# Performance work log

Measured on AMD Instinct MI355X. Metric: run time of the kernel, lower is better.

## Reference

```python
import jax, jax.numpy as jnp
import numpy as np
import math

B, S, NV, D, VD = 2, 1024, 256, 4096, 768
H, KV, HD = 32, 4, 128
REP = H // KV
THETA, YSCALE, YALPHA, YBETA = 10000.0, 40.0, 1.0, 32.0
MAXSEQ = 2048
NEG = -1e30


def _yarn_cos_sin(n_pos):
    # YaRN-scaled RoPE tables, faithful to precompute_rope_yarn
    L_full = MAXSEQ * int(YSCALE)  # max_seq_len * yarn_scale as in __init__
    inv_freq = 1.0 / THETA ** (np.arange(0, HD, 2, dtype=np.float32) / HD)
    wavelengths = 2.0 * math.pi / inv_freq
    r = L_full / wavelengths
    gamma = np.clip((r - YALPHA) / (YBETA - YALPHA), 0.0, 1.0)
    inv_freq = inv_freq * ((1.0 - gamma) / YSCALE + gamma)
    freqs = np.outer(np.arange(n_pos, dtype=np.float32), inv_freq)
    emb = np.concatenate([freqs, freqs], axis=-1) / math.sqrt(0.1 * math.log(YSCALE) + 1.0)
    return jnp.asarray(np.cos(emb), jnp.float32), jnp.asarray(np.sin(emb), jnp.float32)


def setup_inputs() -> dict:
    key = jax.random.key(0)
    ks = jax.random.split(key, 7)
    x = jax.random.normal(ks[0], (B, S, D), jnp.float32)
    vision_features = jax.random.normal(ks[1], (B, NV, VD), jnp.float32)
    wq = jax.random.normal(ks[2], (H * HD, D), jnp.float32) * 0.02
    wk = jax.random.normal(ks[3], (KV * HD, D), jnp.float32) * 0.02
    wv = jax.random.normal(ks[4], (KV * HD, D), jnp.float32) * 0.02
    wo = jax.random.normal(ks[5], (D, H * HD), jnp.float32) * 0.02
    w_vision_kv = jax.random.normal(ks[6], (2 * KV * HD, VD), jnp.float32) * 0.02
    cos, sin = _yarn_cos_sin(S + NV)
    return {"x": x, "vision_features": vision_features, "wq": wq, "wk": wk,
            "wv": wv, "wo": wo, "w_vision_kv": w_vision_kv, "cos": cos, "sin": sin}


def _rotate_half(t):
    t1, t2 = t[..., : HD // 2], t[..., HD // 2 :]
    return jnp.concatenate([-t2, t1], axis=-1)


def reference(x, vision_features, wq, wk, wv, wo, w_vision_kv, cos, sin):
    b, s, _ = x.shape
    q = (x @ wq.T).reshape(b, s, H, HD)
    k = (x @ wk.T).reshape(b, s, KV, HD)
    v = (x @ wv.T).reshape(b, s, KV, HD)
    # vision KV prefix
    vkv = vision_features @ w_vision_kv.T  # [b, nv, 2*KV*HD]
    vk, vv = jnp.split(vkv, 2, axis=-1)
    nv = vision_features.shape[1]
    vk = vk.reshape(b, nv, KV, HD)
    vv = vv.reshape(b, nv, KV, HD)
    k = jnp.concatenate([vk, k], axis=1)  # [b, kvlen, KV, HD]
    v = jnp.concatenate([vv, v], axis=1)
    kvlen = k.shape[1]
    # RoPE (positions broadcast over heads)
    cq, sq = cos[None, :s, None, :], sin[None, :s, None, :]
    ck, sk = cos[None, :kvlen, None, :], sin[None, :kvlen, None, :]
    q = q * cq + _rotate_half(q) * sq
    k = k * ck + _rotate_half(k) * sk
    # GQA without materializing repeated K/V: group q heads by kv head
    qg = q.reshape(b, s, KV, REP, HD)
    scores = jnp.einsum("bsgrd,btgd->bgrst", qg, k) * (HD ** -0.5)
    # flash-style bottom-right causal: q pos i sees kv pos j <= i + (kvlen - s)
    i = jnp.arange(s)[:, None]
    j = jnp.arange(kvlen)[None, :]
    mask = j <= i + (kvlen - s)
    scores = jnp.where(mask, scores, NEG)
    probs = jax.nn.softmax(scores, axis=-1)
    out = jnp.einsum("bgrst,btgd->bsgrd", probs, v).reshape(b, s, H * HD)
    return out @ wo.T
```

## Files before the change

kernel.cpp:

```cpp
#include <hip/hip_runtime.h>
#include <hip/hip_bf16.h>
#include <cstdint>
#include <cstddef>

typedef short bf16x8 __attribute__((ext_vector_type(8)));
typedef float f32x4 __attribute__((ext_vector_type(4)));

__device__ __forceinline__ void gload_lds16(const void* g, void* l) {
  __builtin_amdgcn_global_load_lds((__attribute__((address_space(1))) const void*)g,
                                   (__attribute__((address_space(3))) void*)l, 16, 0, 0);
}

__device__ __forceinline__ unsigned short f2bf(float f) {
  unsigned u = __builtin_bit_cast(unsigned, f);
  u += 0x7fffu + ((u >> 16) & 1u);
  return (unsigned short)(u >> 16);
}
__device__ __forceinline__ float bf2f(unsigned short h) {
  unsigned u = ((unsigned)h) << 16;
  return __builtin_bit_cast(float, u);
}

__global__ void k_cast(const float* __restrict__ in, unsigned short* __restrict__ out, int n4) {
  int i = blockIdx.x * blockDim.x + threadIdx.x;
  int stride = gridDim.x * blockDim.x;
  for (; i < n4; i += stride) {
    float4 v = reinterpret_cast<const float4*>(in)[i];
    ushort4 o;
    o.x = f2bf(v.x); o.y = f2bf(v.y); o.z = f2bf(v.z); o.w = f2bf(v.w);
    reinterpret_cast<ushort4*>(out)[i] = o;
  }
}

__device__ __forceinline__ void storeC(float* C, size_t i, float v) { C[i] = v; }
__device__ __forceinline__ void storeC(unsigned short* C, size_t i, float v) { C[i] = f2bf(v); }

template <typename OutT>
__global__ __launch_bounds__(256) void k_gemm_bt(
    const unsigned short* __restrict__ A,
    const unsigned short* __restrict__ B,
    OutT* __restrict__ C,
    int M, int N, int K) {
  __shared__ __align__(16) unsigned short lA[128 * 64];
  __shared__ __align__(16) unsigned short lB[128 * 64];
  const int tid = threadIdx.x;
  const int w = tid >> 6, l = tid & 63;
  const int nwg = gridDim.x * gridDim.y;
  const int orig = blockIdx.y * gridDim.x + blockIdx.x;
  const int cpx = nwg >> 3;
  const int tile = (orig & 7) * cpx + (orig >> 3);
  const int m0 = (tile % gridDim.x) * 128;
  const int n0 = (tile / gridDim.x) * 128;
  const int wm = (w >> 1) * 64, wn = (w & 1) * 64;

  f32x4 acc[4][4];
#pragma unroll
  for (int i = 0; i < 4; ++i)
#pragma unroll
    for (int j = 0; j < 4; ++j) acc[i][j] = f32x4{0.f, 0.f, 0.f, 0.f};

  char* lAc = (char*)lA;
  char* lBc = (char*)lB;

  for (int k0 = 0; k0 < K; k0 += 64) {
#pragma unroll
    for (int p = 0; p < 4; ++p) {
      int r = (w * 4 + p) * 8 + (l >> 3);
      int c = (l & 7) ^ (r & 7);
      gload_lds16(A + (size_t)(m0 + r) * K + k0 + c * 8, lAc + (w * 4 + p) * 1024);
      gload_lds16(B + (size_t)(n0 + r) * K + k0 + c * 8, lBc + (w * 4 + p) * 1024);
    }
    __syncthreads();
#pragma unroll
    for (int kk = 0; kk < 2; ++kk) {
      bf16x8 af[4], bfr[4];
#pragma unroll
      for (int i = 0; i < 4; ++i) {
        int r = wm + i * 16 + (l & 15);
        int slot = (kk * 4 + (l >> 4)) ^ (r & 7);
        af[i] = *(const bf16x8*)(lAc + r * 128 + slot * 16);
      }
#pragma unroll
      for (int j = 0; j < 4; ++j) {
        int r = wn + j * 16 + (l & 15);
        int slot = (kk * 4 + (l >> 4)) ^ (r & 7);
        bfr[j] = *(const bf16x8*)(lBc + r * 128 + slot * 16);
      }
#pragma unroll
      for (int i = 0; i < 4; ++i)
#pragma unroll
        for (int j = 0; j < 4; ++j)
          acc[i][j] = __builtin_amdgcn_mfma_f32_16x16x32_bf16(af[i], bfr[j], acc[i][j], 0, 0, 0);
    }
    __syncthreads();
  }

#pragma unroll
  for (int i = 0; i < 4; ++i)
#pragma unroll
    for (int j = 0; j < 4; ++j) {
      int row = m0 + wm + i * 16 + (l >> 4) * 4;
      int col = n0 + wn + j * 16 + (l & 15);
#pragma unroll
      for (int r = 0; r < 4; ++r)
        storeC(C, (size_t)(row + r) * N + col, acc[i][j][r]);
    }
}

__global__ void k_rope_q(unsigned short* __restrict__ qkv,
                         const float* __restrict__ cosT, const float* __restrict__ sinT) {
  int idx = blockIdx.x * blockDim.x + threadIdx.x;
  if (idx >= 2048 * 32 * 64) return;
  int d0 = idx & 63;
  int h = (idx >> 6) & 31;
  int m = idx >> 11;
  int s = m & 1023;
  unsigned short* row = qkv + (size_t)m * 5120 + h * 128;
  float a = bf2f(row[d0]), b = bf2f(row[d0 + 64]);
  float c0 = cosT[s * 128 + d0], s0 = sinT[s * 128 + d0];
  float c1 = cosT[s * 128 + d0 + 64], s1 = sinT[s * 128 + d0 + 64];
  const float sc = 0.08838834764831845f;
  row[d0] = f2bf((a * c0 - b * s0) * sc);
  row[d0 + 64] = f2bf((b * c1 + a * s1) * sc);
}

__global__ void k_build_k(const unsigned short* __restrict__ qkv,
                          const unsigned short* __restrict__ vkv,
                          const float* __restrict__ cosT, const float* __restrict__ sinT,
                          unsigned short* __restrict__ k_all) {
  int idx = blockIdx.x * blockDim.x + threadIdx.x;
  if (idx >= 8 * 1280 * 64) return;
  int d0 = idx & 63;
  int t = (idx >> 6) % 1280;
  int bg = idx / (64 * 1280);
  int b = bg >> 2, g = bg & 3;
  float a, bb;
  if (t < 256) {
    const unsigned short* src = vkv + (size_t)(b * 256 + t) * 1024 + g * 128;
    a = bf2f(src[d0]); bb = bf2f(src[d0 + 64]);
  } else {
    const unsigned short* src = qkv + (size_t)(b * 1024 + t - 256) * 5120 + 4096 + g * 128;
    a = bf2f(src[d0]); bb = bf2f(src[d0 + 64]);
  }
  float c0 = cosT[t * 128 + d0], s0 = sinT[t * 128 + d0];
  float c1 = cosT[t * 128 + d0 + 64], s1 = sinT[t * 128 + d0 + 64];
  unsigned short* dst = k_all + ((size_t)bg * 1280 + t) * 128;
  dst[d0] = f2bf(a * c0 - bb * s0);
  dst[d0 + 64] = f2bf(bb * c1 + a * s1);
}

__global__ void k_build_v(const unsigned short* __restrict__ qkv,
                          const unsigned short* __restrict__ vkv,
                          unsigned short* __restrict__ v_t) {
  int idx = blockIdx.x * blockDim.x + threadIdx.x;
  if (idx >= 8 * 128 * 1280) return;
  int t = idx % 1280;
  int d = (idx / 1280) & 127;
  int bg = idx / (1280 * 128);
  int b = bg >> 2, g = bg & 3;
  unsigned short v;
  if (t < 256) v = vkv[(size_t)(b * 256 + t) * 1024 + 512 + g * 128 + d];
  else         v = qkv[(size_t)(b * 1024 + t - 256) * 5120 + 4608 + g * 128 + d];
  v_t[(size_t)bg * 128 * 1280 + (size_t)d * 1280 + t] = v;
}

__global__ __launch_bounds__(256) void k_attn(
    const unsigned short* __restrict__ qr,
    const unsigned short* __restrict__ k_all,
    const unsigned short* __restrict__ v_t,
    unsigned short* __restrict__ attn) {
  __shared__ __align__(16) unsigned short lK[2][64 * 128];
  __shared__ __align__(16) unsigned short lV[2][128 * 64];
  __shared__ __align__(16) unsigned short lPT[4][16][64];

  const int tid = threadIdx.x, w = tid >> 6, l = tid & 63;
  const int lq = l & 15, g = l >> 4;
  const int qb = (15 - (int)blockIdx.x) * 64;
  const int h = blockIdx.y, b = blockIdx.z;
  const int bg = b * 4 + (h >> 3);
  const unsigned short* kg = k_all + (size_t)bg * 1280 * 128;
  const unsigned short* vg = v_t + (size_t)bg * 128 * 1280;

  char* lKc = (char*)lK;
  char* lVc = (char*)lV;
  char* pbuf = (char*)&lPT[w][0][0];

  bf16x8 aq[4];
  {
    int row = qb + w * 16 + lq;
    const unsigned short* p = qr + (size_t)(b * 1024 + row) * 5120 + h * 128 + g * 8;
    aq[0] = *(const bf16x8*)(p);
    aq[1] = *(const bf16x8*)(p + 32);
    aq[2] = *(const bf16x8*)(p + 64);
    aq[3] = *(const bf16x8*)(p + 96);
  }

  f32x4 o[8];
#pragma unroll
  for (int i = 0; i < 8; ++i) o[i] = f32x4{0.f, 0.f, 0.f, 0.f};
  float mr = -1e30f;
  float lrp = 0.f;

  const int qrow_l = qb + w * 16 + lq;
  int tlim = qb + 320;
  if (tlim > 1280) tlim = 1280;
  const int nIter = tlim >> 6;

  auto stage = [&](int t0, int bufsel) {
#pragma unroll
    for (int p = 0; p < 4; ++p) {
      int r = (w * 4 + p) * 4 + (l >> 4);
      int c = (l & 15) ^ (r & 7);
      gload_lds16(kg + (size_t)(t0 + r) * 128 + c * 8,
                  lKc + bufsel * 16384 + (w * 4 + p) * 1024);
    }
#pragma unroll
    for (int p = 0; p < 4; ++p) {
      int d = (w * 4 + p) * 8 + (l >> 3);
      int c = (l & 7) ^ (d & 7);
      gload_lds16(vg + (size_t)d * 1280 + t0 + c * 8,
                  lVc + bufsel * 16384 + (w * 4 + p) * 1024);
    }
  };

  stage(0, 0);
  __syncthreads();

  int buf = 0;
  for (int it = 0; it < nIter; ++it) {
    const int t0 = it << 6;
    if (it + 1 < nIter) stage(t0 + 64, buf ^ 1);

    const char* kbase = lKc + buf * 16384;
    const char* vbase = lVc + buf * 16384;

    f32x4 sT[4];
#pragma unroll
    for (int sub = 0; sub < 4; ++sub) {
      f32x4 s4 = {0.f, 0.f, 0.f, 0.f};
      int krow = sub * 16 + lq;
      const char* kb = kbase + krow * 256;
#pragma unroll
      for (int kk = 0; kk < 4; ++kk) {
        int slot = (kk * 4 + g) ^ (krow & 7);
        bf16x8 kf = *(const bf16x8*)(kb + slot * 16);
        s4 = __builtin_amdgcn_mfma_f32_16x16x32_bf16(kf, aq[kk], s4, 0, 0, 0);
      }
      sT[sub] = s4;
    }

    if (t0 + 63 > qb + w * 16 + 256) {
#pragma unroll
      for (int sub = 0; sub < 4; ++sub)
#pragma unroll
        for (int r = 0; r < 4; ++r) {
          int t = t0 + sub * 16 + 4 * g + r;
          if (t > qrow_l + 256) sT[sub][r] = -1e30f;
        }
    }

    float pm = fmaxf(fmaxf(fmaxf(sT[0][0], sT[0][1]), fmaxf(sT[0][2], sT[0][3])),
                     fmaxf(fmaxf(sT[1][0], sT[1][1]), fmaxf(sT[1][2], sT[1][3])));
    pm = fmaxf(pm, fmaxf(fmaxf(fmaxf(sT[2][0], sT[2][1]), fmaxf(sT[2][2], sT[2][3])),
                         fmaxf(fmaxf(sT[3][0], sT[3][1]), fmaxf(sT[3][2], sT[3][3]))));
    pm = fmaxf(pm, __shfl_xor(pm, 16));
    pm = fmaxf(pm, __shfl_xor(pm, 32));

    if (!__all(pm <= mr + 8.0f)) {
      float mnew = fmaxf(mr, pm);
      float scl = __expf(mr - mnew);
      mr = mnew;
      lrp *= scl;
      float s0 = __shfl(scl, 4 * g + 0);
      float s1 = __shfl(scl, 4 * g + 1);
      float s2 = __shfl(scl, 4 * g + 2);
      float s3 = __shfl(scl, 4 * g + 3);
#pragma unroll
      for (int cs = 0; cs < 8; ++cs) {
        o[cs][0] *= s0; o[cs][1] *= s1; o[cs][2] *= s2; o[cs][3] *= s3;
      }
    }

#pragma unroll
    for (int sub = 0; sub < 4; ++sub) {
      float p0 = __expf(sT[sub][0] - mr);
      float p1 = __expf(sT[sub][1] - mr);
      float p2 = __expf(sT[sub][2] - mr);
      float p3 = __expf(sT[sub][3] - mr);
      lrp += (p0 + p1) + (p2 + p3);
      unsigned pk0, pk1;
      asm("v_cvt_pk_bf16_f32 %0, %1, %2" : "=v"(pk0) : "v"(p0), "v"(p1));
      asm("v_cvt_pk_bf16_f32 %0, %1, %2" : "=v"(pk1) : "v"(p2), "v"(p3));
      int c = (2 * sub + (g >> 1)) ^ (lq & 7);
      *(uint2*)(pbuf + lq * 128 + c * 16 + (g & 1) * 8) = make_uint2(pk0, pk1);
    }

    asm volatile("s_waitcnt lgkmcnt(0)" ::: "memory");
    __builtin_amdgcn_sched_barrier(0);

    bf16x8 pa0 = *(const bf16x8*)(pbuf + lq * 128 + ((g ^ (lq & 7)) * 16));
    bf16x8 pa1 = *(const bf16x8*)(pbuf + lq * 128 + (((4 + g) ^ (lq & 7)) * 16));

#pragma unroll
    for (int cs = 0; cs < 8; ++cs) {
      int drow = cs * 16 + lq;
      const char* vb = vbase + drow * 128;
      int s0i = g ^ (drow & 7);
      int s1i = (4 + g) ^ (drow & 7);
      bf16x8 v0 = *(const bf16x8*)(vb + s0i * 16);
      bf16x8 v1 = *(const bf16x8*)(vb + s1i * 16);
      o[cs] = __builtin_amdgcn_mfma_f32_16x16x32_bf16(pa0, v0, o[cs], 0, 0, 0);
      o[cs] = __builtin_amdgcn_mfma_f32_16x16x32_bf16(pa1, v1, o[cs], 0, 0, 0);
    }

    __syncthreads();
    buf ^= 1;
  }

  lrp += __shfl_xor(lrp, 16);
  lrp += __shfl_xor(lrp, 32);
  float inv = 1.0f / lrp;
  float invr[4];
  invr[0] = __shfl(inv, 4 * g + 0);
  invr[1] = __shfl(inv, 4 * g + 1);
  invr[2] = __shfl(inv, 4 * g + 2);
  invr[3] = __shfl(inv, 4 * g + 3);
#pragma unroll
  for (int cs = 0; cs < 8; ++cs)
#pragma unroll
    for (int r = 0; r < 4; ++r) {
      int row = qb + w * 16 + 4 * g + r;
      attn[(size_t)(b * 1024 + row) * 4096 + h * 128 + cs * 16 + lq] =
          f2bf(o[cs][r] * invr[r]);
    }
}

extern "C" void kernel_launch(void* const* d_in, const int* in_sizes, int n_in,
                              void* d_out, int out_size, void* d_ws, size_t ws_size,
                              hipStream_t stream) {
  const float* x    = (const float*)d_in[0];
  const float* vis  = (const float*)d_in[1];
  const float* wq   = (const float*)d_in[2];
  const float* wk   = (const float*)d_in[3];
  const float* wv   = (const float*)d_in[4];
  const float* wo   = (const float*)d_in[5];
  const float* wvkv = (const float*)d_in[6];
  const float* cosT = (const float*)d_in[7];
  const float* sinT = (const float*)d_in[8];
  float* out = (float*)d_out;
  char* ws = (char*)d_ws;

  size_t off = 0;
  auto alloc = [&](size_t b) { size_t r = off; off += (b + 255) & ~(size_t)255; return r; };
  unsigned short* wqkvb = (unsigned short*)(ws + alloc((size_t)5120 * 4096 * 2));
  unsigned short* wob   = (unsigned short*)(ws + alloc((size_t)4096 * 4096 * 2));
  unsigned short* wvkvb = (unsigned short*)(ws + alloc((size_t)1024 * 768 * 2));
  unsigned short* visb  = (unsigned short*)(ws + alloc((size_t)512 * 768 * 2));
  unsigned short* xb    = (unsigned short*)(ws + alloc((size_t)2048 * 4096 * 2));
  unsigned short* qkv   = (unsigned short*)(ws + alloc((size_t)2048 * 5120 * 2));
  unsigned short* vkvb  = (unsigned short*)(ws + alloc((size_t)512 * 1024 * 2));
  unsigned short* kall  = (unsigned short*)(ws + alloc((size_t)8 * 1280 * 128 * 2));
  unsigned short* vt    = (unsigned short*)(ws + alloc((size_t)8 * 128 * 1280 * 2));
  unsigned short* attnb = xb;
  if (ws_size < off) return;

  auto cast = [&](const float* src, unsigned short* dst, size_t n) {
    int n4 = (int)(n / 4);
    int grid = (n4 + 255) / 256;
    if (grid > 1280) grid = 1280;
    k_cast<<<dim3(grid), dim3(256), 0, stream>>>(src, dst, n4);
  };
  cast(x, xb, (size_t)2048 * 4096);
  cast(wq, wqkvb, (size_t)4096 * 4096);
  cast(wk, wqkvb + (size_t)4096 * 4096, (size_t)512 * 4096);
  cast(wv, wqkvb + (size_t)4608 * 4096, (size_t)512 * 4096);
  cast(wo, wob, (size_t)4096 * 4096);
  cast(wvkv, wvkvb, (size_t)1024 * 768);
  cast(vis, visb, (size_t)512 * 768);

  k_gemm_bt<unsigned short><<<dim3(16, 40), dim3(256), 0, stream>>>(xb, wqkvb, qkv, 2048, 5120, 4096);
  k_gemm_bt<unsigned short><<<dim3(4, 8), dim3(256), 0, stream>>>(visb, wvkvb, vkvb, 512, 1024, 768);

  k_rope_q<<<dim3(16384), dim3(256), 0, stream>>>(qkv, cosT, sinT);
  k_build_k<<<dim3(2560), dim3(256), 0, stream>>>(qkv, vkvb, cosT, sinT, kall);
  k_build_v<<<dim3(5120), dim3(256), 0, stream>>>(qkv, vkvb, vt);

  k_attn<<<dim3(16, 32, 2), dim3(256), 0, stream>>>(qkv, kall, vt, attnb);

  k_gemm_bt<float><<<dim3(16, 32), dim3(256), 0, stream>>>(attnb, wob, out, 2048, 4096, 4096);
}
```

Measured before the change: 358.6 us.

## Add 256x256-tile 8-wave pipelined GEMM for QKV and output projections

Adds a new bf16 MFMA GEMM kernel that uses 256x256 output tiles with 512 threads, double-buffered swizzled LDS fed by direct global-to-LDS loads, and phase-split MFMA blocks with barriers and priority hints. Block indices are remapped so tiles are grouped per XCD. The QKV and output projections switch from the 128-tile kernel to this one, aiming for more operand reuse and overlap of loads with compute. The grids are small (160 and 128 blocks on a GPU with roughly 256 CUs), so occupancy and wave quantisation may suffer, and the index mapping assumes the exact problem shapes.

```diff
diff --git a/kernel.cpp b/kernel.cpp
--- a/kernel.cpp
+++ b/kernel.cpp
@@ -107,6 +107,147 @@
     }
 }
 
+#define READ_B4(bf, kh)                                                        \
+  {                                                                            \
+    bfr[0] = *(const bf16x8*)&lB[bf][kh][wc * 64 + 0 * 16 + lq][fslot];        \
+    bfr[1] = *(const bf16x8*)&lB[bf][kh][wc * 64 + 1 * 16 + lq][fslot];        \
+    bfr[2] = *(const bf16x8*)&lB[bf][kh][wc * 64 + 2 * 16 + lq][fslot];        \
+    bfr[3] = *(const bf16x8*)&lB[bf][kh][wc * 64 + 3 * 16 + lq][fslot];        \
+  }
+#define READ_A4(bf, kh, mfb)                                                   \
+  {                                                                            \
+    a[0] = *(const bf16x8*)&lA[bf][kh][wr * 128 + ((mfb) + 0) * 16 + lq][fslot];\
+    a[1] = *(const bf16x8*)&lA[bf][kh][wr * 128 + ((mfb) + 1) * 16 + lq][fslot];\
+    a[2] = *(const bf16x8*)&lA[bf][kh][wr * 128 + ((mfb) + 2) * 16 + lq][fslot];\
+    a[3] = *(const bf16x8*)&lA[bf][kh][wr * 128 + ((mfb) + 3) * 16 + lq][fslot];\
+  }
+#define MFMA16(mfb)                                                            \
+  _Pragma("unroll") for (int i = 0; i < 4; ++i)                                \
+      _Pragma("unroll") for (int nf = 0; nf < 4; ++nf)                         \
+          acc[(mfb) + i][nf] = __builtin_amdgcn_mfma_f32_16x16x32_bf16(        \
+              a[i], bfr[nf], acc[(mfb) + i][nf], 0, 0, 0);
+#define PHASE_SYNC_PRE()                         \
+  __builtin_amdgcn_sched_barrier(0);             \
+  __builtin_amdgcn_s_barrier();                  \
+  asm volatile("s_waitcnt lgkmcnt(0)" ::: "memory"); \
+  __builtin_amdgcn_sched_barrier(0);             \
+  __builtin_amdgcn_s_setprio(1);
+#define PHASE_SYNC_POST()                        \
+  __builtin_amdgcn_s_setprio(0);                 \
+  __builtin_amdgcn_sched_barrier(0);             \
+  __builtin_amdgcn_s_barrier();                  \
+  __builtin_amdgcn_sched_barrier(0);
+
+template <typename OutT>
+__global__ __launch_bounds__(512) void k_gemm256(
+    const unsigned short* __restrict__ A,
+    const unsigned short* __restrict__ B,
+    OutT* __restrict__ C,
+    int M, int N, int K) {
+  __shared__ __align__(16) unsigned short lA[2][2][256][32];
+  __shared__ __align__(16) unsigned short lB[2][2][256][32];
+  const int tid = threadIdx.x;
+  const int w = tid >> 6, l = tid & 63;
+  const int wr = w >> 2, wc = w & 3;
+  const int lq = l & 15, g = l >> 4;
+  const int fslot = (g ^ ((lq >> 1) & 3)) << 3;
+
+  const int gy = (int)gridDim.x >> 3;
+  const int L = (int)blockIdx.x;
+  const int xcd = L & 7, slot = L >> 3;
+  const int m0 = ((xcd >> 2) * 4 + (slot & 3)) * 256;
+  const int n0 = ((xcd & 3) * (gy >> 2) + (slot >> 2)) * 256;
+
+  const unsigned short* Ap = A + (size_t)m0 * K;
+  const unsigned short* Bp = B + (size_t)n0 * K;
+
+  f32x4 acc[8][4];
+#pragma unroll
+  for (int i = 0; i < 8; ++i)
+#pragma unroll
+    for (int j = 0; j < 4; ++j) acc[i][j] = f32x4{0.f, 0.f, 0.f, 0.f};
+
+  auto stageHT = [&](const unsigned short* gbase, unsigned short* lbase, int kcol) {
+#pragma unroll
+    for (int p = 0; p < 2; ++p) {
+      int R = w * 32 + p * 16;
+      int row = R + (l >> 2);
+      int cc = ((l & 3) ^ ((l >> 3) & 3)) << 3;
+      gload_lds16(gbase + (size_t)row * K + kcol + cc, lbase + R * 32);
+    }
+  };
+
+  const int nt = K >> 6;
+
+  stageHT(Bp, &lB[0][0][0][0], 0);
+  stageHT(Ap, &lA[0][0][0][0], 0);
+  stageHT(Bp, &lB[0][1][0][0], 32);
+  stageHT(Ap, &lA[0][1][0][0], 32);
+  stageHT(Bp, &lB[1][0][0][0], 64);
+  stageHT(Ap, &lA[1][0][0][0], 64);
+  stageHT(Bp, &lB[1][1][0][0], 96);
+  asm volatile("s_waitcnt vmcnt(6)" ::: "memory");
+  __builtin_amdgcn_s_barrier();
+  __builtin_amdgcn_sched_barrier(0);
+
+  bf16x8 bfr[4], a[4];
+
+  for (int T = 0; T < nt; ++T) {
+    const int bf = T & 1, nb = bf ^ 1;
+    const int kc2 = (T + 2) << 6;
+    unsigned short (*lAb)[256][32] = lA[bf];
+    unsigned short (*lBb)[256][32] = lB[bf];
+
+    READ_B4(bf, 0);
+    READ_A4(bf, 0, 0);
+    if (T + 1 < nt) stageHT(Ap, &lA[nb][1][0][0], ((T + 1) << 6) + 32);
+    PHASE_SYNC_PRE();
+    MFMA16(0);
+    PHASE_SYNC_POST();
+
+    READ_A4(bf, 0, 4);
+    if (T + 2 < nt) stageHT(Bp, &lBb[0][0][0], kc2);
+    PHASE_SYNC_PRE();
+    MFMA16(4);
+    PHASE_SYNC_POST();
+
+    READ_B4(bf, 1);
+    READ_A4(bf, 1, 0);
+    if (T + 2 < nt) stageHT(Ap, &lAb[0][0][0], kc2);
+    PHASE_SYNC_PRE();
+    MFMA16(0);
+    PHASE_SYNC_POST();
+
+    READ_A4(bf, 1, 4);
+    if (T + 2 < nt) stageHT(Bp, &lBb[1][0][0], kc2 + 32);
+    __builtin_amdgcn_sched_barrier(0);
+    __builtin_amdgcn_s_barrier();
+    asm volatile("s_waitcnt lgkmcnt(0)" ::: "memory");
+    __builtin_amdgcn_sched_barrier(0);
+    __builtin_amdgcn_s_setprio(1);
+    MFMA16(4);
+    __builtin_amdgcn_s_setprio(0);
+    __builtin_amdgcn_sched_barrier(0);
+    if (T < nt - 2)
+      asm volatile("s_waitcnt vmcnt(6)" ::: "memory");
+    else if (T == nt - 2)
+      asm volatile("s_waitcnt vmcnt(0)" ::: "memory");
+    __builtin_amdgcn_s_barrier();
+    __builtin_amdgcn_sched_barrier(0);
+  }
+
+#pragma unroll
+  for (int mf = 0; mf < 8; ++mf)
+#pragma unroll
+    for (int nf = 0; nf < 4; ++nf) {
+      int row = m0 + wr * 128 + mf * 16 + g * 4;
+      int col = n0 + wc * 64 + nf * 16 + lq;
+#pragma unroll
+      for (int r = 0; r < 4; ++r)
+        storeC(C, (size_t)(row + r) * N + col, acc[mf][nf][r]);
+    }
+}
+
 __global__ void k_rope_q(unsigned short* __restrict__ qkv,
                          const float* __restrict__ cosT, const float* __restrict__ sinT) {
   int idx = blockIdx.x * blockDim.x + threadIdx.x;
@@ -378,7 +519,7 @@
   cast(wvkv, wvkvb, (size_t)1024 * 768);
   cast(vis, visb, (size_t)512 * 768);
 
-  k_gemm_bt<unsigned short><<<dim3(16, 40), dim3(256), 0, stream>>>(xb, wqkvb, qkv, 2048, 5120, 4096);
+  k_gemm256<unsigned short><<<dim3(160), dim3(512), 0, stream>>>(xb, wqkvb, qkv, 2048, 5120, 4096);
   k_gemm_bt<unsigned short><<<dim3(4, 8), dim3(256), 0, stream>>>(visb, wvkvb, vkvb, 512, 1024, 768);
 
   k_rope_q<<<dim3(16384), dim3(256), 0, stream>>>(qkv, cosT, sinT);
@@ -387,5 +528,5 @@
 
   k_attn<<<dim3(16, 32, 2), dim3(256), 0, stream>>>(qkv, kall, vt, attnb);
 
-  k_gemm_bt<float><<<dim3(16, 32), dim3(256), 0, stream>>>(attnb, wob, out, 2048, 4096, 4096);
-}
+  k_gemm256<float><<<dim3(128), dim3(512), 0, stream>>>(attnb, wob, out, 2048, 4096, 4096);
+}
```

New measurement: 403.2 us. 1.12x slower.

## Fuse cast launches and add pipelined 256x128 GEMM for output projection

Applied to the files above, without the earlier changes.

Merges the seven separate fp32-to-bf16 cast launches into one kernel that walks all segments, removing per-launch overhead. Adds a new 512-thread 256x128-tile GEMM for the output projection. It double-buffers LDS with split-K half stages, uses async global-to-LDS loads with explicit vmcnt waits and barriers, raises wave priority during MFMA phases, and maps tiles to XCDs. The new GEMM depends on M, N and K matching the tiling assumptions and uses more LDS and registers per block.

```diff
diff --git a/kernel.cpp b/kernel.cpp
--- a/kernel.cpp
+++ b/kernel.cpp
@@ -21,14 +21,25 @@
   return __builtin_bit_cast(float, u);
 }
 
-__global__ void k_cast(const float* __restrict__ in, unsigned short* __restrict__ out, int n4) {
-  int i = blockIdx.x * blockDim.x + threadIdx.x;
-  int stride = gridDim.x * blockDim.x;
-  for (; i < n4; i += stride) {
-    float4 v = reinterpret_cast<const float4*>(in)[i];
-    ushort4 o;
-    o.x = f2bf(v.x); o.y = f2bf(v.y); o.z = f2bf(v.z); o.w = f2bf(v.w);
-    reinterpret_cast<ushort4*>(out)[i] = o;
+struct CastPack {
+  const float* s[7];
+  unsigned short* d[7];
+  int n4[7];
+};
+__global__ void k_cast_all(CastPack p) {
+  const int tid0 = blockIdx.x * blockDim.x + threadIdx.x;
+  const int stride = gridDim.x * blockDim.x;
+#pragma unroll 1
+  for (int seg = 0; seg < 7; ++seg) {
+    const float4* __restrict__ src = reinterpret_cast<const float4*>(p.s[seg]);
+    ushort4* __restrict__ dst = reinterpret_cast<ushort4*>(p.d[seg]);
+    const int n4 = p.n4[seg];
+    for (int i = tid0; i < n4; i += stride) {
+      float4 v = src[i];
+      ushort4 o;
+      o.x = f2bf(v.x); o.y = f2bf(v.y); o.z = f2bf(v.z); o.w = f2bf(v.w);
+      dst[i] = o;
+    }
   }
 }
 
@@ -104,6 +115,131 @@
 #pragma unroll
       for (int r = 0; r < 4; ++r)
         storeC(C, (size_t)(row + r) * N + col, acc[i][j][r]);
+    }
+}
+
+#define PHASE_SYNC_PRE()                         \
+  __builtin_amdgcn_sched_barrier(0);             \
+  __builtin_amdgcn_s_barrier();                  \
+  asm volatile("s_waitcnt lgkmcnt(0)" ::: "memory"); \
+  __builtin_amdgcn_sched_barrier(0);             \
+  __builtin_amdgcn_s_setprio(1);
+#define PHASE_SYNC_POST()                        \
+  __builtin_amdgcn_s_setprio(0);                 \
+  __builtin_amdgcn_sched_barrier(0);             \
+  __builtin_amdgcn_s_barrier();                  \
+  __builtin_amdgcn_sched_barrier(0);
+#define XREAD_B2(bf, kh)                                                     \
+  bfr[0] = *(const bf16x8*)&lB[bf][kh][wc * 32 + 0 + lq][fslot];             \
+  bfr[1] = *(const bf16x8*)&lB[bf][kh][wc * 32 + 16 + lq][fslot];
+#define XREAD_A8(bf, kh)                                                     \
+  _Pragma("unroll") for (int mf = 0; mf < 8; ++mf)                           \
+      a[mf] = *(const bf16x8*)&lA[bf][kh][wr * 128 + mf * 16 + lq][fslot];
+#define XMFMA16()                                                            \
+  _Pragma("unroll") for (int mf = 0; mf < 8; ++mf)                           \
+      _Pragma("unroll") for (int nf = 0; nf < 2; ++nf)                       \
+          acc[mf][nf] = __builtin_amdgcn_mfma_f32_16x16x32_bf16(             \
+              a[mf], bfr[nf], acc[mf][nf], 0, 0, 0);
+
+template <typename OutT>
+__global__ __launch_bounds__(512) void k_gemm256x128(
+    const unsigned short* __restrict__ A,
+    const unsigned short* __restrict__ B,
+    OutT* __restrict__ C,
+    int M, int N, int K) {
+  __shared__ __align__(16) unsigned short lA[2][2][256][32];
+  __shared__ __align__(16) unsigned short lB[2][2][128][32];
+  const int tid = threadIdx.x;
+  const int w = tid >> 6, l = tid & 63;
+  const int wr = w >> 2, wc = w & 3;
+  const int lq = l & 15, g = l >> 4;
+  const int fslot = (g ^ ((lq >> 1) & 3)) << 3;
+
+  const int gm = M >> 8, gn = N >> 7;
+  const int L = (int)blockIdx.x;
+  const int xcd = L & 7, slot = L >> 3;
+  const int m0 = (slot % gm) * 256;
+  const int n0 = (xcd * (gn >> 3) + slot / gm) * 128;
+
+  const unsigned short* Ap = A + (size_t)m0 * K;
+  const unsigned short* Bp = B + (size_t)n0 * K;
+
+  f32x4 acc[8][2];
+#pragma unroll
+  for (int i = 0; i < 8; ++i)
+#pragma unroll
+    for (int j = 0; j < 2; ++j) acc[i][j] = f32x4{0.f, 0.f, 0.f, 0.f};
+
+  auto stageA = [&](unsigned short* lbase, int kcol) {
+#pragma unroll
+    for (int p = 0; p < 2; ++p) {
+      int R = w * 32 + p * 16;
+      int row = R + (l >> 2);
+      int cc = ((l & 3) ^ ((l >> 3) & 3)) << 3;
+      gload_lds16(Ap + (size_t)row * K + kcol + cc, lbase + R * 32);
+    }
+  };
+  auto stageB = [&](unsigned short* lbase, int kcol) {
+    int R = w * 16;
+    int row = R + (l >> 2);
+    int cc = ((l & 3) ^ ((l >> 3) & 3)) << 3;
+    gload_lds16(Bp + (size_t)row * K + kcol + cc, lbase + R * 32);
+  };
+
+  const int nt = K >> 6;
+
+  stageB(&lB[0][0][0][0], 0);
+  stageA(&lA[0][0][0][0], 0);
+  stageB(&lB[0][1][0][0], 32);
+  stageA(&lA[0][1][0][0], 32);
+  stageB(&lB[1][0][0][0], 64);
+  stageA(&lA[1][0][0][0], 64);
+  asm volatile("s_waitcnt vmcnt(3)" ::: "memory");
+  __builtin_amdgcn_s_barrier();
+  __builtin_amdgcn_sched_barrier(0);
+
+  bf16x8 bfr[2], a[8];
+
+  for (int T = 0; T < nt; ++T) {
+    const int bf = T & 1, nb = bf ^ 1;
+
+    XREAD_B2(bf, 0);
+    XREAD_A8(bf, 0);
+    if (T + 1 < nt) {
+      stageA(&lA[nb][1][0][0], ((T + 1) << 6) + 32);
+      stageB(&lB[nb][1][0][0], ((T + 1) << 6) + 32);
+    }
+    PHASE_SYNC_PRE();
+    XMFMA16();
+    PHASE_SYNC_POST();
+
+    XREAD_B2(bf, 1);
+    XREAD_A8(bf, 1);
+    if (T + 2 < nt) {
+      stageA(&lA[bf][0][0][0], (T + 2) << 6);
+      stageB(&lB[bf][0][0][0], (T + 2) << 6);
+    }
+    PHASE_SYNC_PRE();
+    XMFMA16();
+    __builtin_amdgcn_s_setprio(0);
+    __builtin_amdgcn_sched_barrier(0);
+    if (T < nt - 2)
+      asm volatile("s_waitcnt vmcnt(3)" ::: "memory");
+    else if (T == nt - 2)
+      asm volatile("s_waitcnt vmcnt(0)" ::: "memory");
+    __builtin_amdgcn_s_barrier();
+    __builtin_amdgcn_sched_barrier(0);
+  }
+
+#pragma unroll
+  for (int mf = 0; mf < 8; ++mf)
+#pragma unroll
+    for (int nf = 0; nf < 2; ++nf) {
+      int row = m0 + wr * 128 + mf * 16 + g * 4;
+      int col = n0 + wc * 32 + nf * 16 + lq;
+#pragma unroll
+      for (int r = 0; r < 4; ++r)
+        storeC(C, (size_t)(row + r) * N + col, acc[mf][nf][r]);
     }
 }
 
@@ -364,19 +500,15 @@
   unsigned short* attnb = xb;
   if (ws_size < off) return;
 
-  auto cast = [&](const float* src, unsigned short* dst, size_t n) {
-    int n4 = (int)(n / 4);
-    int grid = (n4 + 255) / 256;
-    if (grid > 1280) grid = 1280;
-    k_cast<<<dim3(grid), dim3(256), 0, stream>>>(src, dst, n4);
-  };
-  cast(x, xb, (size_t)2048 * 4096);
-  cast(wq, wqkvb, (size_t)4096 * 4096);
-  cast(wk, wqkvb + (size_t)4096 * 4096, (size_t)512 * 4096);
-  cast(wv, wqkvb + (size_t)4608 * 4096, (size_t)512 * 4096);
-  cast(wo, wob, (size_t)4096 * 4096);
-  cast(wvkv, wvkvb, (size_t)1024 * 768);
-  cast(vis, visb, (size_t)512 * 768);
+  CastPack cp;
+  cp.s[0] = x;    cp.d[0] = xb;                           cp.n4[0] = 2048 * 4096 / 4;
+  cp.s[1] = wq;   cp.d[1] = wqkvb;                        cp.n4[1] = 4096 * 4096 / 4;
+  cp.s[2] = wk;   cp.d[2] = wqkvb + (size_t)4096 * 4096;  cp.n4[2] = 512 * 4096 / 4;
+  cp.s[3] = wv;   cp.d[3] = wqkvb + (size_t)4608 * 4096;  cp.n4[3] = 512 * 4096 / 4;
+  cp.s[4] = wo;   cp.d[4] = wob;                          cp.n4[4] = 4096 * 4096 / 4;
+  cp.s[5] = wvkv; cp.d[5] = wvkvb;                        cp.n4[5] = 1024 * 768 / 4;
+  cp.s[6] = vis;  cp.d[6] = visb;                         cp.n4[6] = 512 * 768 / 4;
+  k_cast_all<<<dim3(2048), dim3(256), 0, stream>>>(cp);
 
   k_gemm_bt<unsigned short><<<dim3(16, 40), dim3(256), 0, stream>>>(xb, wqkvb, qkv, 2048, 5120, 4096);
   k_gemm_bt<unsigned short><<<dim3(4, 8), dim3(256), 0, stream>>>(visb, wvkvb, vkvb, 512, 1024, 768);
@@ -387,5 +519,5 @@
 
   k_attn<<<dim3(16, 32, 2), dim3(256), 0, stream>>>(qkv, kall, vt, attnb);
 
-  k_gemm_bt<float><<<dim3(16, 32), dim3(256), 0, stream>>>(attnb, wob, out, 2048, 4096, 4096);
-}
+  k_gemm256x128<float><<<dim3(256), dim3(512), 0, stream>>>(attnb, wob, out, 2048, 4096, 4096);
+}
```

After: 353.8 us. Within noise of the previous version (-1.3%).
